# Optimization experiments

Hardware: AMD Instinct MI355X
Metric: run time of the kernel (lower is better)

The kernel has to match this reference:

```python
import jax, jax.numpy as jnp
import numpy as np

B, S, D, H = 2, 2048, 1024, 16
DH = D // H  # 64


def setup_inputs() -> dict:
    key = jax.random.key(0)
    k1, k2, k3 = jax.random.split(key, 3)
    return {
        "x": jax.random.normal(k1, (B, S, D), dtype=jnp.float32),
        "w_qkv": jax.random.normal(k2, (D, 3 * D), dtype=jnp.float32) * 0.02,
        "b_qkv": jnp.zeros((3 * D,), dtype=jnp.float32),
        "w_out": jax.random.normal(k3, (D, D), dtype=jnp.float32) * 0.02,
        "b_out": jnp.zeros((D,), dtype=jnp.float32),
    }


def reference(x, w_qkv, b_qkv, w_out, b_out):
    # fused qkv projection: [B,S,3D]
    qkv = x @ w_qkv + b_qkv
    q, k, v = qkv[..., :D], qkv[..., D:2 * D], qkv[..., 2 * D:]
    # split heads -> [B,H,S,DH]
    split = lambda t: t.reshape(B, S, H, DH).transpose(0, 2, 1, 3)
    q, k, v = split(q), split(k), split(v)
    scale = 1.0 / jnp.sqrt(jnp.asarray(DH, dtype=x.dtype))
    scores = jnp.einsum("bhqd,bhkd->bhqk", q, k) * scale  # [B,H,S,S]
    attn = jax.nn.softmax(scores, axis=-1)
    out = jnp.einsum("bhqk,bhkd->bhqd", attn, v)  # [B,H,S,DH]
    out = out.transpose(0, 2, 1, 3).reshape(B, S, D)
    return out @ w_out + b_out
```

## Files before the change

### kernel.cpp

```cpp
#include <hip/hip_runtime.h>
#include <cstdint>

#define B_ 2
#define S_ 2048
#define D_ 1024
#define H_ 16
#define DH_ 64

typedef short bf16x8 __attribute__((ext_vector_type(8)));
typedef float f32x4 __attribute__((ext_vector_type(4)));

__device__ inline unsigned short f2bf(float f) {
  unsigned int u = __float_as_uint(f);
  u += 0x7fffu + ((u >> 16) & 1u);
  return (unsigned short)(u >> 16);
}

__device__ inline float bf2f(unsigned short h) {
  return __uint_as_float(((unsigned int)h) << 16);
}

__device__ inline float fexp2(float x) { return __builtin_amdgcn_exp2f(x); }

__device__ inline int swz(int row, int bytecol) {
  return row * 128 + (bytecol ^ ((row & 7) << 4));
}

#define GLL(gp, lp)                                                            \
  __builtin_amdgcn_global_load_lds(                                            \
      (const __attribute__((address_space(1))) unsigned int*)(gp),             \
      (__attribute__((address_space(3))) unsigned int*)(lp), 16, 0, 0)

__global__ __launch_bounds__(256) void k_cast(const float* __restrict__ in,
                                              unsigned short* __restrict__ out, int n4) {
  int i = blockIdx.x * 256 + threadIdx.x;
  if (i >= n4) return;
  float4 v = reinterpret_cast<const float4*>(in)[i];
  ushort4 o;
  o.x = f2bf(v.x); o.y = f2bf(v.y); o.z = f2bf(v.z); o.w = f2bf(v.w);
  reinterpret_cast<ushort4*>(out)[i] = o;
}

__global__ __launch_bounds__(256) void k_trcast(const float* __restrict__ in,
                                                unsigned short* __restrict__ out,
                                                int R, int C) {
  __shared__ float tile[32][33];
  int ct = blockIdx.x * 32, rt = blockIdx.y * 32;
  int tx = threadIdx.x, ty = threadIdx.y;
#pragma unroll
  for (int i = 0; i < 32; i += 8)
    tile[ty + i][tx] = in[(size_t)(rt + ty + i) * C + ct + tx];
  __syncthreads();
#pragma unroll
  for (int i = 0; i < 32; i += 8)
    out[(size_t)(ct + ty + i) * R + rt + tx] = f2bf(tile[tx][ty + i]);
}

template <typename OutT>
__global__ __launch_bounds__(256) void k_gemm(const unsigned short* __restrict__ A,
                                              const unsigned short* __restrict__ BT,
                                              const float* __restrict__ bias,
                                              OutT* __restrict__ C,
                                              unsigned short* __restrict__ VTout,
                                              int M, int N, int K) {
  __shared__ unsigned short As[128 * 64];
  __shared__ unsigned short Bs[128 * 64];
  const int t = threadIdx.x;
  const int lane = t & 63;
  const int wave = t >> 6;
  const int wm = wave >> 1, wn = wave & 1;
  const int ln15 = lane & 15, lg = lane >> 4;
  const int row0 = blockIdx.x * 128, col0 = blockIdx.y * 128;
  f32x4 acc[4][4];
#pragma unroll
  for (int i = 0; i < 4; ++i)
#pragma unroll
    for (int j = 0; j < 4; ++j)
      acc[i][j] = (f32x4){0.f, 0.f, 0.f, 0.f};

  for (int k0 = 0; k0 < K; k0 += 64) {
    __syncthreads();
#pragma unroll
    for (int i = 0; i < 4; ++i) {
      int chunk = i * 256 + t;
      int r = chunk >> 3;
      int cb = (chunk & 7) * 16;
      const char* ga = (const char*)(A + (size_t)(row0 + r) * K + k0) + cb;
      const char* gb = (const char*)(BT + (size_t)(col0 + r) * K + k0) + cb;
      GLL(ga, (char*)As + chunk * 16);
      GLL(gb, (char*)Bs + chunk * 16);
    }
    __syncthreads();
#pragma unroll
    for (int ks = 0; ks < 2; ++ks) {
      bf16x8 af[4], bf[4];
#pragma unroll
      for (int mt = 0; mt < 4; ++mt)
        af[mt] = *(const bf16x8*)&As[(wm * 64 + mt * 16 + ln15) * 64 + ks * 32 + lg * 8];
#pragma unroll
      for (int nt = 0; nt < 4; ++nt)
        bf[nt] = *(const bf16x8*)&Bs[(wn * 64 + nt * 16 + ln15) * 64 + ks * 32 + lg * 8];
#pragma unroll
      for (int mt = 0; mt < 4; ++mt)
#pragma unroll
        for (int nt = 0; nt < 4; ++nt)
          acc[mt][nt] = __builtin_amdgcn_mfma_f32_16x16x32_bf16(af[mt], bf[nt], acc[mt][nt], 0, 0, 0);
    }
  }
#pragma unroll
  for (int mt = 0; mt < 4; ++mt) {
#pragma unroll
    for (int nt = 0; nt < 4; ++nt) {
      int col = col0 + wn * 64 + nt * 16 + ln15;
      float bv = bias[col];
      if (VTout != nullptr && col >= 2048) {
        int hd = col - 2048;
        int row = row0 + wm * 64 + mt * 16 + lg * 4;
        int bb = row >> 11, ss = row & 2047;
        ushort4 o;
        o.x = f2bf(acc[mt][nt][0] + bv);
        o.y = f2bf(acc[mt][nt][1] + bv);
        o.z = f2bf(acc[mt][nt][2] + bv);
        o.w = f2bf(acc[mt][nt][3] + bv);
        *(ushort4*)&VTout[(((size_t)(bb * 16 + (hd >> 6)) * 64) + (hd & 63)) * 2048 + ss] = o;
      } else {
#pragma unroll
        for (int r = 0; r < 4; ++r) {
          int row = row0 + wm * 64 + mt * 16 + lg * 4 + r;
          float v = acc[mt][nt][r] + bv;
          if constexpr (sizeof(OutT) == 2)
            C[(size_t)row * N + col] = f2bf(v);
          else
            C[(size_t)row * N + col] = v;
        }
      }
    }
  }
}

__global__ __launch_bounds__(512) void k_attn(const unsigned short* __restrict__ qkv,
                                              const unsigned short* __restrict__ VT,
                                              unsigned short* __restrict__ O) {
  __shared__ unsigned short Ks[2][64 * 64];
  __shared__ unsigned short Vs[2][64 * 64];
  __shared__ unsigned short Ps[8][16 * 64];

  const int bid = blockIdx.x;
  const int xcd = bid & 7, idx = bid >> 3;
  const int bh = xcd + (idx >> 4) * 8;
  const int qblk = idx & 15;
  const int b = bh >> 4, h = bh & 15;
  const int t = threadIdx.x, wave = t >> 6, lane = t & 63;
  const int ln15 = lane & 15, lg = lane >> 4;
  const unsigned short* Qb = qkv + (size_t)b * S_ * 3072 + h * 64;
  const unsigned short* Kb = Qb + 1024;
  const unsigned short* Vb = VT + (size_t)bh * 64 * 2048;
  const int q0 = qblk * 128 + wave * 16;

  const float qsc = 0.125f * 1.4426950408889634f;
  bf16x8 qf[2];
#pragma unroll
  for (int ks = 0; ks < 2; ++ks) {
    bf16x8 raw = *(const bf16x8*)&Qb[(size_t)(q0 + ln15) * 3072 + ks * 32 + lg * 8];
#pragma unroll
    for (int j = 0; j < 8; ++j)
      qf[ks][j] = (short)f2bf(bf2f((unsigned short)raw[j]) * qsc);
  }

  auto stage = [&](int bi, int kv) {
    int row = t >> 3, col = t & 7;
    int gcol = col ^ (row & 7);
    GLL((const char*)(Kb + (size_t)(kv + row) * 3072 + gcol * 8),
        (char*)&Ks[bi][0] + t * 16);
    GLL((const char*)(Vb + (size_t)row * 2048 + kv + gcol * 8),
        (char*)&Vs[bi][0] + t * 16);
  };

  f32x4 acc[4];
#pragma unroll
  for (int dt = 0; dt < 4; ++dt)
    acc[dt] = (f32x4){0.f, 0.f, 0.f, 0.f};
  float m0 = -1e30f, l0 = 0.f;
  unsigned short* Pw = Ps[wave];

  stage(0, 0);
  __syncthreads();
  int buf = 0;

  for (int kv = 0; kv < S_; kv += 64) {
    if (kv + 64 < S_) stage(buf ^ 1, kv + 64);

    f32x4 st[4];
#pragma unroll
    for (int kg = 0; kg < 4; ++kg)
      st[kg] = (f32x4){0.f, 0.f, 0.f, 0.f};
#pragma unroll
    for (int kg = 0; kg < 4; ++kg) {
      int krow = kg * 16 + ln15;
      bf16x8 kf0 = *(const bf16x8*)((const char*)&Ks[buf][0] + swz(krow, lg * 16));
      bf16x8 kf1 = *(const bf16x8*)((const char*)&Ks[buf][0] + swz(krow, 64 + lg * 16));
      st[kg] = __builtin_amdgcn_mfma_f32_16x16x32_bf16(kf0, qf[0], st[kg], 0, 0, 0);
      st[kg] = __builtin_amdgcn_mfma_f32_16x16x32_bf16(kf1, qf[1], st[kg], 0, 0, 0);
    }

    float tm = -1e30f;
#pragma unroll
    for (int kg = 0; kg < 4; ++kg)
      tm = fmaxf(tm, fmaxf(fmaxf(st[kg][0], st[kg][1]),
                           fmaxf(st[kg][2], st[kg][3])));
    tm = fmaxf(tm, __shfl_xor(tm, 16));
    tm = fmaxf(tm, __shfl_xor(tm, 32));

    if (__any(tm > m0 + 11.0f)) {
      float n0 = fmaxf(m0, tm);
      float r0 = fexp2(m0 - n0);
      m0 = n0; l0 *= r0;
#pragma unroll
      for (int dt = 0; dt < 4; ++dt)
#pragma unroll
        for (int r = 0; r < 4; ++r)
          acc[dt][r] *= r0;
    }

    asm volatile("" ::: "memory");
    float ts = 0.f;
#pragma unroll
    for (int kg = 0; kg < 4; ++kg) {
      float p0 = fexp2(st[kg][0] - m0);
      float p1 = fexp2(st[kg][1] - m0);
      float p2 = fexp2(st[kg][2] - m0);
      float p3 = fexp2(st[kg][3] - m0);
      ts += (p0 + p1) + (p2 + p3);
      unsigned int w0, w1;
      asm("v_cvt_pk_bf16_f32 %0, %1, %2" : "=v"(w0) : "v"(p0), "v"(p1));
      asm("v_cvt_pk_bf16_f32 %0, %1, %2" : "=v"(w1) : "v"(p2), "v"(p3));
      *(uint2*)((char*)Pw + swz(ln15, kg * 32 + lg * 8)) = make_uint2(w0, w1);
    }
    ts += __shfl_xor(ts, 16);
    ts += __shfl_xor(ts, 32);
    l0 += ts;
    asm volatile("" ::: "memory");

#pragma unroll
    for (int kc = 0; kc < 2; ++kc) {
      bf16x8 pf = *(const bf16x8*)((const char*)Pw + swz(ln15, kc * 64 + lg * 16));
#pragma unroll
      for (int dt = 0; dt < 4; ++dt) {
        bf16x8 vf = *(const bf16x8*)((const char*)&Vs[buf][0] + swz(dt * 16 + ln15, kc * 64 + lg * 16));
        acc[dt] = __builtin_amdgcn_mfma_f32_16x16x32_bf16(vf, pf, acc[dt], 0, 0, 0);
      }
    }
    __syncthreads();
    buf ^= 1;
  }

  float inv = 1.f / l0;
  size_t qglob = q0 + ln15;
  size_t base = ((size_t)b * S_ + qglob) * D_ + h * 64 + lg * 4;
#pragma unroll
  for (int dt = 0; dt < 4; ++dt) {
    ushort4 o;
    o.x = f2bf(acc[dt][0] * inv);
    o.y = f2bf(acc[dt][1] * inv);
    o.z = f2bf(acc[dt][2] * inv);
    o.w = f2bf(acc[dt][3] * inv);
    *(ushort4*)&O[base + (size_t)dt * 16] = o;
  }
}

extern "C" void kernel_launch(void* const* d_in, const int* in_sizes, int n_in,
                              void* d_out, int out_size, void* d_ws, size_t ws_size,
                              hipStream_t stream) {
  const float* x     = (const float*)d_in[0];
  const float* w_qkv = (const float*)d_in[1];
  const float* b_qkv = (const float*)d_in[2];
  const float* w_out = (const float*)d_in[3];
  const float* b_out = (const float*)d_in[4];
  float* out = (float*)d_out;

  char* ws = (char*)d_ws;
  const size_t MiB = (size_t)1 << 20;
  unsigned short* xb   = (unsigned short*)(ws + 0 * MiB);
  unsigned short* wqT  = (unsigned short*)(ws + 8 * MiB);
  unsigned short* woT  = (unsigned short*)(ws + 14 * MiB);
  unsigned short* qkvb = (unsigned short*)(ws + 16 * MiB);
  unsigned short* VTb  = (unsigned short*)(ws + 40 * MiB);
  unsigned short* Ab   = (unsigned short*)(ws + 48 * MiB);

  k_cast<<<4096, 256, 0, stream>>>(x, xb, (B_ * S_ * D_) / 4);
  k_trcast<<<dim3(96, 32), dim3(32, 8), 0, stream>>>(w_qkv, wqT, 1024, 3072);
  k_trcast<<<dim3(32, 32), dim3(32, 8), 0, stream>>>(w_out, woT, 1024, 1024);
  k_gemm<unsigned short><<<dim3(32, 24), 256, 0, stream>>>(xb, wqT, b_qkv, qkvb, VTb, 4096, 3072, 1024);
  k_attn<<<512, 512, 0, stream>>>(qkvb, VTb, Ab);
  k_gemm<float><<<dim3(32, 8), 256, 0, stream>>>(Ab, woT, b_out, out, nullptr, 4096, 1024, 1024);
}
```

Measured before the change: 217.6 us.

## Template GEMM tiles, add XCD-aware block swizzle, setprio and hoisted staging in attention

```diff
diff --git a/kernel.cpp b/kernel.cpp
--- a/kernel.cpp
+++ b/kernel.cpp
@@ -56,66 +56,75 @@
     out[(size_t)(ct + ty + i) * R + rt + tx] = f2bf(tile[tx][ty + i]);
 }
 
-template <typename OutT>
+template <int BM, int BN, typename OutT>
 __global__ __launch_bounds__(256) void k_gemm(const unsigned short* __restrict__ A,
                                               const unsigned short* __restrict__ BT,
                                               const float* __restrict__ bias,
                                               OutT* __restrict__ C,
                                               unsigned short* __restrict__ VTout,
                                               int M, int N, int K) {
-  __shared__ unsigned short As[128 * 64];
-  __shared__ unsigned short Bs[128 * 64];
+  constexpr int MT = BM / 32, NT = BN / 32;
+  __shared__ unsigned short As[BM * 64];
+  __shared__ unsigned short Bs[BN * 64];
   const int t = threadIdx.x;
   const int lane = t & 63;
   const int wave = t >> 6;
   const int wm = wave >> 1, wn = wave & 1;
   const int ln15 = lane & 15, lg = lane >> 4;
-  const int row0 = blockIdx.x * 128, col0 = blockIdx.y * 128;
-  f32x4 acc[4][4];
-#pragma unroll
-  for (int i = 0; i < 4; ++i)
-#pragma unroll
-    for (int j = 0; j < 4; ++j)
+  const int nwg = gridDim.x * gridDim.y;
+  const int flat = blockIdx.y * gridDim.x + blockIdx.x;
+  const int cpx = nwg >> 3;
+  const int sid = (flat & 7) * cpx + (flat >> 3);
+  const int row0 = (sid % gridDim.x) * BM, col0 = (sid / gridDim.x) * BN;
+  f32x4 acc[MT][NT];
+#pragma unroll
+  for (int i = 0; i < MT; ++i)
+#pragma unroll
+    for (int j = 0; j < NT; ++j)
       acc[i][j] = (f32x4){0.f, 0.f, 0.f, 0.f};
 
   for (int k0 = 0; k0 < K; k0 += 64) {
     __syncthreads();
 #pragma unroll
-    for (int i = 0; i < 4; ++i) {
+    for (int i = 0; i < BM / 32; ++i) {
       int chunk = i * 256 + t;
       int r = chunk >> 3;
       int cb = (chunk & 7) * 16;
-      const char* ga = (const char*)(A + (size_t)(row0 + r) * K + k0) + cb;
-      const char* gb = (const char*)(BT + (size_t)(col0 + r) * K + k0) + cb;
-      GLL(ga, (char*)As + chunk * 16);
-      GLL(gb, (char*)Bs + chunk * 16);
+      GLL((const char*)(A + (size_t)(row0 + r) * K + k0) + cb, (char*)As + chunk * 16);
+    }
+#pragma unroll
+    for (int i = 0; i < BN / 32; ++i) {
+      int chunk = i * 256 + t;
+      int r = chunk >> 3;
+      int cb = (chunk & 7) * 16;
+      GLL((const char*)(BT + (size_t)(col0 + r) * K + k0) + cb, (char*)Bs + chunk * 16);
     }
     __syncthreads();
 #pragma unroll
     for (int ks = 0; ks < 2; ++ks) {
-      bf16x8 af[4], bf[4];
-#pragma unroll
-      for (int mt = 0; mt < 4; ++mt)
-        af[mt] = *(const bf16x8*)&As[(wm * 64 + mt * 16 + ln15) * 64 + ks * 32 + lg * 8];
-#pragma unroll
-      for (int nt = 0; nt < 4; ++nt)
-        bf[nt] = *(const bf16x8*)&Bs[(wn * 64 + nt * 16 + ln15) * 64 + ks * 32 + lg * 8];
-#pragma unroll
-      for (int mt = 0; mt < 4; ++mt)
-#pragma unroll
-        for (int nt = 0; nt < 4; ++nt)
+      bf16x8 af[MT], bf[NT];
+#pragma unroll
+      for (int mt = 0; mt < MT; ++mt)
+        af[mt] = *(const bf16x8*)&As[(wm * (BM / 2) + mt * 16 + ln15) * 64 + ks * 32 + lg * 8];
+#pragma unroll
+      for (int nt = 0; nt < NT; ++nt)
+        bf[nt] = *(const bf16x8*)&Bs[(wn * (BN / 2) + nt * 16 + ln15) * 64 + ks * 32 + lg * 8];
+#pragma unroll
+      for (int mt = 0; mt < MT; ++mt)
+#pragma unroll
+        for (int nt = 0; nt < NT; ++nt)
           acc[mt][nt] = __builtin_amdgcn_mfma_f32_16x16x32_bf16(af[mt], bf[nt], acc[mt][nt], 0, 0, 0);
     }
   }
 #pragma unroll
-  for (int mt = 0; mt < 4; ++mt) {
-#pragma unroll
-    for (int nt = 0; nt < 4; ++nt) {
-      int col = col0 + wn * 64 + nt * 16 + ln15;
+  for (int mt = 0; mt < MT; ++mt) {
+#pragma unroll
+    for (int nt = 0; nt < NT; ++nt) {
+      int col = col0 + wn * (BN / 2) + nt * 16 + ln15;
       float bv = bias[col];
       if (VTout != nullptr && col >= 2048) {
         int hd = col - 2048;
-        int row = row0 + wm * 64 + mt * 16 + lg * 4;
+        int row = row0 + wm * (BM / 2) + mt * 16 + lg * 4;
         int bb = row >> 11, ss = row & 2047;
         ushort4 o;
         o.x = f2bf(acc[mt][nt][0] + bv);
@@ -126,7 +135,7 @@
       } else {
 #pragma unroll
         for (int r = 0; r < 4; ++r) {
-          int row = row0 + wm * 64 + mt * 16 + lg * 4 + r;
+          int row = row0 + wm * (BM / 2) + mt * 16 + lg * 4 + r;
           float v = acc[mt][nt][r] + bv;
           if constexpr (sizeof(OutT) == 2)
             C[(size_t)row * N + col] = f2bf(v);
@@ -167,13 +176,16 @@
       qf[ks][j] = (short)f2bf(bf2f((unsigned short)raw[j]) * qsc);
   }
 
+  const int srow = t >> 3;
+  const int scol = (t & 7) ^ (srow & 7);
+  const unsigned short* kPtr0 = Kb + (size_t)srow * 3072 + scol * 8;
+  const unsigned short* vPtr0 = Vb + (size_t)srow * 2048 + scol * 8;
+  char* ldsK0 = (char*)&Ks[0][0] + t * 16;
+  char* ldsV0 = (char*)&Vs[0][0] + t * 16;
+
   auto stage = [&](int bi, int kv) {
-    int row = t >> 3, col = t & 7;
-    int gcol = col ^ (row & 7);
-    GLL((const char*)(Kb + (size_t)(kv + row) * 3072 + gcol * 8),
-        (char*)&Ks[bi][0] + t * 16);
-    GLL((const char*)(Vb + (size_t)row * 2048 + kv + gcol * 8),
-        (char*)&Vs[bi][0] + t * 16);
+    GLL(kPtr0 + (size_t)kv * 3072, ldsK0 + bi * 8192);
+    GLL(vPtr0 + kv, ldsV0 + bi * 8192);
   };
 
   f32x4 acc[4];
@@ -194,6 +206,7 @@
 #pragma unroll
     for (int kg = 0; kg < 4; ++kg)
       st[kg] = (f32x4){0.f, 0.f, 0.f, 0.f};
+    __builtin_amdgcn_s_setprio(1);
 #pragma unroll
     for (int kg = 0; kg < 4; ++kg) {
       int krow = kg * 16 + ln15;
@@ -202,6 +215,7 @@
       st[kg] = __builtin_amdgcn_mfma_f32_16x16x32_bf16(kf0, qf[0], st[kg], 0, 0, 0);
       st[kg] = __builtin_amdgcn_mfma_f32_16x16x32_bf16(kf1, qf[1], st[kg], 0, 0, 0);
     }
+    __builtin_amdgcn_s_setprio(0);
 
     float tm = -1e30f;
 #pragma unroll
@@ -241,6 +255,7 @@
     l0 += ts;
     asm volatile("" ::: "memory");
 
+    __builtin_amdgcn_s_setprio(1);
 #pragma unroll
     for (int kc = 0; kc < 2; ++kc) {
       bf16x8 pf = *(const bf16x8*)((const char*)Pw + swz(ln15, kc * 64 + lg * 16));
@@ -250,6 +265,7 @@
         acc[dt] = __builtin_amdgcn_mfma_f32_16x16x32_bf16(vf, pf, acc[dt], 0, 0, 0);
       }
     }
+    __builtin_amdgcn_s_setprio(0);
     __syncthreads();
     buf ^= 1;
   }
@@ -290,7 +306,7 @@
   k_cast<<<4096, 256, 0, stream>>>(x, xb, (B_ * S_ * D_) / 4);
   k_trcast<<<dim3(96, 32), dim3(32, 8), 0, stream>>>(w_qkv, wqT, 1024, 3072);
   k_trcast<<<dim3(32, 32), dim3(32, 8), 0, stream>>>(w_out, woT, 1024, 1024);
-  k_gemm<unsigned short><<<dim3(32, 24), 256, 0, stream>>>(xb, wqT, b_qkv, qkvb, VTb, 4096, 3072, 1024);
+  k_gemm<128, 128, unsigned short><<<dim3(32, 24), 256, 0, stream>>>(xb, wqT, b_qkv, qkvb, VTb, 4096, 3072, 1024);
   k_attn<<<512, 512, 0, stream>>>(qkvb, VTb, Ab);
-  k_gemm<float><<<dim3(32, 8), 256, 0, stream>>>(Ab, woT, b_out, out, nullptr, 4096, 1024, 1024);
-}
+  k_gemm<64, 64, float><<<dim3(64, 16), 256, 0, stream>>>(Ab, woT, b_out, out, nullptr, 4096, 1024, 1024);
+}
```

Measured after the change: 215.6 us. Within noise of the previous version (-0.9%).
